# Kernel optimization log

Hardware: AMD Instinct MI355X
Metric: run time of the kernel (lower is better)

The kernel has to match this reference:

```python
import jax, jax.numpy as jnp
import numpy as np

TWN_THRESHOLD_FACTOR = 0.05
BN_EPS = 1e-5


def ternary_quantize(w):
    # threshold = 0.05 * max|w| (detached); q in {-1, 0, +1}
    t = TWN_THRESHOLD_FACTOR * jnp.max(jnp.abs(jax.lax.stop_gradient(w)))
    return (w > t).astype(w.dtype) - (w < -t).astype(w.dtype)


def conv2d(x, w, b):
    q = ternary_quantize(w)
    y = jax.lax.conv_general_dilated(x, q, (1, 1), 'VALID',
                                     dimension_numbers=('NCHW', 'OIHW', 'NCHW'))
    return y + b[None, :, None, None]


def linear(x, w, b):
    q = ternary_quantize(w)
    return x @ q.T + b


def bn_train(x, gamma, beta, axes):
    # training-mode batch norm (biased variance), matches torch BN in train()
    mean = jnp.mean(x, axis=axes, keepdims=True)
    var = jnp.var(x, axis=axes, keepdims=True)
    xhat = (x - mean) * jax.lax.rsqrt(var + BN_EPS)
    shape = [1] * x.ndim
    shape[1] = x.shape[1]
    return xhat * gamma.reshape(shape) + beta.reshape(shape)


def maxpool2(x):
    return jax.lax.reduce_window(x, -jnp.inf, jax.lax.max,
                                 (1, 1, 2, 2), (1, 1, 2, 2), 'VALID')


def setup_inputs() -> dict:
    key = jax.random.key(0)
    ks = jax.random.split(key, 8)
    B, Cin, H, W = 512, 1, 28, 28
    C1, C2, K = 64, 128, 5
    FLAT, F1, F2 = 4 * 4 * C2, 512, 10
    inp = {
        'x': jax.random.normal(ks[0], (B, Cin, H, W), jnp.float32),
        'conv1_w': jax.random.normal(ks[1], (C1, Cin, K, K), jnp.float32) * (1.0 / np.sqrt(Cin * K * K)),
        'conv1_b': jax.random.normal(ks[2], (C1,), jnp.float32) * 0.05,
        'bn1_g': jnp.ones((C1,), jnp.float32),
        'bn1_b': jnp.zeros((C1,), jnp.float32),
        'conv2_w': jax.random.normal(ks[3], (C2, C1, K, K), jnp.float32) * (1.0 / np.sqrt(C1 * K * K)),
        'conv2_b': jax.random.normal(ks[4], (C2,), jnp.float32) * 0.05,
        'bn2_g': jnp.ones((C2,), jnp.float32),
        'bn2_b': jnp.zeros((C2,), jnp.float32),
        'fc1_w': jax.random.normal(ks[5], (F1, FLAT), jnp.float32) * (1.0 / np.sqrt(FLAT)),
        'fc1_b': jax.random.normal(ks[6], (F1,), jnp.float32) * 0.05,
        'bn3_g': jnp.ones((F1,), jnp.float32),
        'bn3_b': jnp.zeros((F1,), jnp.float32),
        'fc2_w': jax.random.normal(ks[7], (F2, F1), jnp.float32) * (1.0 / np.sqrt(F1)),
        'fc2_b': jnp.zeros((F2,), jnp.float32),
    }
    return inp


def reference(x, conv1_w, conv1_b, bn1_g, bn1_b, conv2_w, conv2_b, bn2_g, bn2_b,
              fc1_w, fc1_b, bn3_g, bn3_b, fc2_w, fc2_b):
    h = jax.nn.relu(bn_train(conv2d(x, conv1_w, conv1_b), bn1_g, bn1_b, (0, 2, 3)))
    h = maxpool2(h)  # [B, 64, 12, 12]
    h = jax.nn.relu(bn_train(conv2d(h, conv2_w, conv2_b), bn2_g, bn2_b, (0, 2, 3)))
    h = maxpool2(h)  # [B, 128, 4, 4]
    h = h.reshape(h.shape[0], -1)  # [B, 2048]
    h = jax.nn.relu(bn_train(linear(h, fc1_w, fc1_b), bn3_g, bn3_b, (0,)))
    return linear(h, fc2_w, fc2_b)  # [B, 10]
```

## Files before the change

### kernel.cpp

```cpp
#include <hip/hip_runtime.h>
#include <stdint.h>

#define EPS 1e-5f

typedef short v8s __attribute__((ext_vector_type(8)));
typedef float v4f __attribute__((ext_vector_type(4)));

static const size_t W1F  = 4096;
static const size_t W2F  = 8192;
static const size_t WF2F = 212992;
static const size_t A_F  = 262144;
static const size_t B_F  = 19136512;
static const size_t WF1T = B_F + 1048576;

__device__ inline unsigned short f2bf(float f) {
    unsigned u = __float_as_uint(f);
    return (unsigned short)((u + 0x7FFF + ((u >> 16) & 1)) >> 16);
}

__device__ __forceinline__ void stage16(const unsigned short* g, unsigned short* l) {
    __builtin_amdgcn_global_load_lds(
        (const __attribute__((address_space(1))) unsigned int*)g,
        (__attribute__((address_space(3))) unsigned int*)l, 16, 0, 0);
}

__global__ void k_zero(float* p, int n) {
    int i = blockIdx.x * blockDim.x + threadIdx.x;
    if (i < n) p[i] = 0.f;
}

__global__ void k_absmax4(const float* __restrict__ w0, int n0,
                          const float* __restrict__ w1, int n1,
                          const float* __restrict__ w2, int n2,
                          const float* __restrict__ w3, int n3,
                          float* outv) {
    int blk = blockIdx.x;
    const float* w; int n; unsigned* out; int nb; int bi;
    if (blk < 1)        { w = w0; n = n0; out = (unsigned*)(outv + 0); nb = 1;   bi = blk;      }
    else if (blk < 17)  { w = w1; n = n1; out = (unsigned*)(outv + 1); nb = 16;  bi = blk - 1;  }
    else if (blk < 209) { w = w2; n = n2; out = (unsigned*)(outv + 2); nb = 192; bi = blk - 17; }
    else                { w = w3; n = n3; out = (unsigned*)(outv + 3); nb = 1;   bi = blk - 209; }
    float m = 0.f;
    for (int i = bi * 256 + threadIdx.x; i < n; i += nb * 256)
        m = fmaxf(m, fabsf(w[i]));
    #pragma unroll
    for (int o = 32; o; o >>= 1) m = fmaxf(m, __shfl_down(m, o));
    if ((threadIdx.x & 63) == 0) atomicMax(out, __float_as_uint(m));
}

__global__ void k_quantE(const float* __restrict__ c1w, const float* __restrict__ c2w,
                         const float* __restrict__ f2w, const float* __restrict__ am,
                         float* __restrict__ w1t, unsigned short* __restrict__ w2u,
                         float* __restrict__ wf2) {
    int blk = blockIdx.x;
    if (blk < 1) {
        float t = 0.05f * am[0];
        for (int i = threadIdx.x; i < 1600; i += 256) {
            float v = c1w[i];
            float q = (float)((v > t) - (v < -t));
            int c = i / 25, k = i - c * 25;
            w1t[k * 64 + c] = q;
        }
    } else if (blk < 101) {
        float t = 0.05f * am[1];
        int base = (blk - 1) * 2048;
        #pragma unroll
        for (int jj = 0; jj < 8; ++jj) {
            int i = base + jj * 256 + threadIdx.x;
            int j    = i & 7;
            int lane = (i >> 3) & 63;
            int mt   = (i >> 9) & 7;
            int ks   = (i >> 12) & 1;
            int p    = i >> 13;
            int c  = mt * 16 + (lane & 15);
            int ci = ks * 32 + (lane >> 4) * 8 + j;
            float v = c2w[c * 1600 + ci * 25 + p];
            w2u[i] = (v > t) ? (unsigned short)0x3F80
                             : ((v < -t) ? (unsigned short)0xBF80 : (unsigned short)0);
        }
    } else {
        float t = 0.05f * am[3];
        for (int i = threadIdx.x; i < 5120; i += 256) {
            float v = f2w[i];
            wf2[i] = (float)((v > t) - (v < -t));
        }
    }
}

__global__ void k_quantF1(const float* __restrict__ w, const float* __restrict__ am,
                          unsigned short* __restrict__ wf) {
    float t = 0.05f * am[2];
    int i = blockIdx.x * 256 + threadIdx.x;
    int j    = i & 7;
    int lane = (i >> 3) & 63;
    int ft   = (i >> 9) & 31;
    int ks   = i >> 14;
    int f = ft * 16 + (lane & 15);
    int k = ks * 32 + (lane >> 4) * 8 + j;
    float v = w[f * 2048 + k];
    wf[i] = (v > t) ? (unsigned short)0x3F80
                    : ((v < -t) ? (unsigned short)0xBF80 : (unsigned short)0);
}

__global__ __launch_bounds__(512) void k_conv1(const float* __restrict__ x,
                                               const float* __restrict__ w1t,
                                               unsigned* __restrict__ pmn1,
                                               float* __restrict__ sum,
                                               float* __restrict__ ssq) {
    __shared__ float xs[784];
    __shared__ float red[2][8][64];
    int b = blockIdx.x;
    const float4* xim = (const float4*)(x + (size_t)b * 784);
    for (int i = threadIdx.x; i < 196; i += 512) ((float4*)xs)[i] = xim[i];
    int c  = threadIdx.x & 63;
    int wv = threadIdx.x >> 6;
    float w[25];
    #pragma unroll
    for (int k = 0; k < 25; ++k) w[k] = w1t[k * 64 + c];
    __syncthreads();
    unsigned* ob = pmn1 + (size_t)b * 9216;
    float s = 0.f, s2 = 0.f;
    int ph = 0, pw = wv;
    for (int it = 0; it < 18; ++it) {
        const float* xp = xs + (ph * 2) * 28 + pw * 2;
        float win[36];
        #pragma unroll
        for (int i = 0; i < 6; ++i)
            #pragma unroll
            for (int j = 0; j < 3; ++j) {
                float2 t2 = *(const float2*)(xp + i * 28 + j * 2);
                win[i * 6 + j * 2] = t2.x; win[i * 6 + j * 2 + 1] = t2.y;
            }
        float v00 = 0.f, v01 = 0.f, v10 = 0.f, v11 = 0.f;
        #pragma unroll
        for (int i = 0; i < 5; ++i)
            #pragma unroll
            for (int j = 0; j < 5; ++j) {
                float wk = w[i * 5 + j];
                v00 = fmaf(win[i * 6 + j],           wk, v00);
                v01 = fmaf(win[i * 6 + j + 1],       wk, v01);
                v10 = fmaf(win[(i + 1) * 6 + j],     wk, v10);
                v11 = fmaf(win[(i + 1) * 6 + j + 1], wk, v11);
            }
        s  += v00 + v01 + v10 + v11;
        s2 += v00 * v00 + v01 * v01 + v10 * v10 + v11 * v11;
        float mx = fmaxf(fmaxf(v00, v01), fmaxf(v10, v11));
        float mn = fminf(fminf(v00, v01), fminf(v10, v11));
        ob[(ph * 12 + pw) * 64 + c] = ((unsigned)f2bf(mx) << 16) | (unsigned)f2bf(mn);
        pw += 8; if (pw >= 12) { pw -= 12; ++ph; }
    }
    red[0][wv][c] = s; red[1][wv][c] = s2;
    __syncthreads();
    if (threadIdx.x < 64) {
        float S = 0.f, S2 = 0.f;
        #pragma unroll
        for (int i = 0; i < 8; ++i) { S += red[0][i][threadIdx.x]; S2 += red[1][i][threadIdx.x]; }
        atomicAdd(&sum[threadIdx.x], S);
        atomicAdd(&ssq[threadIdx.x], S2);
    }
}

__global__ void k_bnpool1(const unsigned* __restrict__ pmn1,
                          const float* __restrict__ c1sum, const float* __restrict__ c1ssq,
                          const float* __restrict__ g1, const float* __restrict__ b1,
                          unsigned short* __restrict__ pool1) {
    int i = blockIdx.x * 256 + threadIdx.x;
    int c = i & 63;
    const float invN = 1.f / 294912.f;
    float mean = c1sum[c] * invN;
    float var  = c1ssq[c] * invN - mean * mean;
    float sc = g1[c] * rsqrtf(var + EPS);
    float sh = b1[c] - mean * sc;
    unsigned u = pmn1[i];
    float mx = __uint_as_float(u & 0xffff0000u);
    float mn = __uint_as_float(u << 16);
    float v = (sc > 0.f) ? mx : mn;
    pool1[i] = f2bf(fmaxf(0.f, fmaf(v, sc, sh)));
}

__global__ __launch_bounds__(256) void k_conv2(const unsigned short* __restrict__ pool1,
                                               const unsigned short* __restrict__ wfrag,
                                               float* __restrict__ pmn,
                                               float* __restrict__ sum,
                                               float* __restrict__ ssq) {
    __shared__ unsigned short xs[144 * 76];
    __shared__ unsigned short wb[2][4096];
    __shared__ float reds[2][64], redq[2][64];
    int b     = blockIdx.x >> 1;
    int mhalf = blockIdx.x & 1;
    int tid  = threadIdx.x;
    int lane = tid & 63;
    int wave = tid >> 6;
    const unsigned short* src = pool1 + (size_t)b * 9216;
    for (int i = tid; i < 1152; i += 256) {
        int r = i >> 3, part = i & 7;
        *(float4*)(&xs[r * 76 + part * 8]) = *(const float4*)(src + r * 64 + part * 8);
    }
    #pragma unroll
    for (int h = 0; h < 2; ++h) {
        const unsigned short* g = wfrag + (size_t)(h * 8 + mhalf * 4 + wave) * 512 + lane * 8;
        stage16(g, &wb[0][h * 2048 + wave * 512 + lane * 8]);
    }
    __syncthreads();

    int mh = wave >> 1, nh = wave & 1;
    int n = lane & 15, quad = lane >> 4;
    int ow = n & 7;
    int ohb0 = nh * 4 + (n >> 3);
    int cib  = quad * 8;
    v4f acc[2][2];
    #pragma unroll
    for (int mm = 0; mm < 2; ++mm) { acc[mm][0] = (v4f){0,0,0,0}; acc[mm][1] = (v4f){0,0,0,0}; }
    for (int ss = 0; ss < 25; ++ss) {
        int cur = ss & 1;
        if (ss < 24) {
            #pragma unroll
            for (int h = 0; h < 2; ++h) {
                int st = 2 * ss + 2 + h;
                const unsigned short* g = wfrag +
                    (size_t)(st * 8 + mhalf * 4 + wave) * 512 + lane * 8;
                stage16(g, &wb[cur ^ 1][h * 2048 + wave * 512 + lane * 8]);
            }
        }
        int kh = ss / 5, kw = ss - (ss / 5) * 5;
        #pragma unroll
        for (int ks = 0; ks < 2; ++ks) {
            int col = (ow + kw) * 76 + ks * 32 + cib;
            v8s bf0 = *(const v8s*)(&xs[(ohb0 + kh) * 912 + col]);
            v8s bf1 = *(const v8s*)(&xs[(ohb0 + 2 + kh) * 912 + col]);
            #pragma unroll
            for (int mm = 0; mm < 2; ++mm) {
                v8s af = *(const v8s*)(&wb[cur][ks * 2048 + (mh * 2 + mm) * 512 + lane * 8]);
                acc[mm][0] = __builtin_amdgcn_mfma_f32_16x16x32_bf16(af, bf0, acc[mm][0], 0, 0, 0);
                acc[mm][1] = __builtin_amdgcn_mfma_f32_16x16x32_bf16(af, bf1, acc[mm][1], 0, 0, 0);
            }
        }
        __syncthreads();
    }
    float* po = pmn + (size_t)b * 4096;
    #pragma unroll
    for (int mm = 0; mm < 2; ++mm) {
        int cl0 = (mh * 2 + mm) * 16 + quad * 4;
        #pragma unroll
        for (int r = 0; r < 4; ++r) {
            int cl = cl0 + r;
            int c  = mhalf * 64 + cl;
            float sA = 0.f, s2A = 0.f;
            #pragma unroll
            for (int bf = 0; bf < 2; ++bf) {
                float v = acc[mm][bf][r];
                float pm = fmaxf(v, __shfl_xor(v, 1));
                float pn = fminf(v, __shfl_xor(v, 1));
                pm = fmaxf(pm, __shfl_xor(pm, 8));
                pn = fminf(pn, __shfl_xor(pn, 8));
                if (((n & 1) == 0) && (n < 8)) {
                    int psp = (nh * 2 + bf) * 4 + (n >> 1);
                    *(float2*)(&po[(c * 16 + psp) * 2]) = make_float2(pm, pn);
                }
                float s = v, s2 = v * v;
                #pragma unroll
                for (int m = 1; m < 16; m <<= 1) { s += __shfl_xor(s, m); s2 += __shfl_xor(s2, m); }
                sA += s; s2A += s2;
            }
            if (n == 0) { reds[nh][cl] = sA; redq[nh][cl] = s2A; }
        }
    }
    __syncthreads();
    if (tid < 64) {
        atomicAdd(&sum[mhalf * 64 + tid], reds[0][tid] + reds[1][tid]);
        atomicAdd(&ssq[mhalf * 64 + tid], redq[0][tid] + redq[1][tid]);
    }
}

__global__ void k_bnpool2(const float* __restrict__ pmn, const float* __restrict__ c2sum,
                          const float* __restrict__ c2ssq, const float* __restrict__ g2,
                          const float* __restrict__ b2, unsigned short* __restrict__ xfrag) {
    int i = blockIdx.x * 256 + threadIdx.x;
    int j    = i & 7;
    int lane = (i >> 3) & 63;
    int bt   = (i >> 9) & 31;
    int ks   = i >> 14;
    int b = bt * 16 + (lane & 15);
    int k = ks * 32 + (lane >> 4) * 8 + j;
    int c = k >> 4, psp = k & 15;
    float2 mm = *(const float2*)(&pmn[((size_t)b * 2048 + c * 16 + psp) * 2]);
    float mean = c2sum[c] * (1.f / 32768.f);
    float var  = c2ssq[c] * (1.f / 32768.f) - mean * mean;
    float sc = g2[c] * rsqrtf(var + EPS);
    float sh = b2[c] - mean * sc;
    float v = (sc > 0.f) ? mm.x : mm.y;
    xfrag[i] = f2bf(fmaxf(0.f, fmaf(v, sc, sh)));
}

__global__ __launch_bounds__(256) void k_fc1(const unsigned short* __restrict__ xfrag,
                                             const unsigned short* __restrict__ wfrag,
                                             float* __restrict__ out,
                                             float* __restrict__ sum,
                                             float* __restrict__ ssq) {
    int lane = threadIdx.x & 63;
    int wave = threadIdx.x >> 6;
    int fB = (blockIdx.x & 3) * 8 + wave * 2;
    int bT = blockIdx.x >> 2;
    v4f acc[2];
    acc[0] = (v4f){0,0,0,0}; acc[1] = (v4f){0,0,0,0};
    for (int ks = 0; ks < 64; ++ks) {
        v8s bfrag = *(const v8s*)(xfrag + ((size_t)(ks * 32 + bT) * 64 + lane) * 8);
        #pragma unroll
        for (int mt = 0; mt < 2; ++mt) {
            v8s afrag = *(const v8s*)(wfrag + ((size_t)(ks * 32 + fB + mt) * 64 + lane) * 8);
            acc[mt] = __builtin_amdgcn_mfma_f32_16x16x32_bf16(afrag, bfrag, acc[mt], 0, 0, 0);
        }
    }
    int bb = bT * 16 + (lane & 15);
    int quad = lane >> 4;
    #pragma unroll
    for (int mt = 0; mt < 2; ++mt) {
        int f0 = (fB + mt) * 16 + quad * 4;
        *(float4*)(&out[(size_t)bb * 512 + f0]) =
            make_float4(acc[mt][0], acc[mt][1], acc[mt][2], acc[mt][3]);
        #pragma unroll
        for (int r = 0; r < 4; ++r) {
            float s = acc[mt][r], s2 = s * s;
            #pragma unroll
            for (int m = 1; m < 16; m <<= 1) { s += __shfl_xor(s, m); s2 += __shfl_xor(s2, m); }
            if ((lane & 15) == 0) { atomicAdd(&sum[f0 + r], s); atomicAdd(&ssq[f0 + r], s2); }
        }
    }
}

__global__ __launch_bounds__(256) void k_fc2(const float* __restrict__ x,
                                             const float* __restrict__ w,
                                             const float* __restrict__ bias,
                                             const float* __restrict__ fsum,
                                             const float* __restrict__ fssq,
                                             const float* __restrict__ g3,
                                             const float* __restrict__ b3,
                                             float* __restrict__ out) {
    int lane = threadIdx.x & 63;
    int b = blockIdx.x * 4 + (threadIdx.x >> 6);
    float xa[8], sm[8], sq[8], ga[8], ba[8];
    {
        const float4* p;
        p = (const float4*)(x + (size_t)b * 512 + lane * 8);
        *(float4*)xa = p[0]; *(float4*)(xa + 4) = p[1];
        p = (const float4*)(fsum + lane * 8);
        *(float4*)sm = p[0]; *(float4*)(sm + 4) = p[1];
        p = (const float4*)(fssq + lane * 8);
        *(float4*)sq = p[0]; *(float4*)(sq + 4) = p[1];
        p = (const float4*)(g3 + lane * 8);
        *(float4*)ga = p[0]; *(float4*)(ga + 4) = p[1];
        p = (const float4*)(b3 + lane * 8);
        *(float4*)ba = p[0]; *(float4*)(ba + 4) = p[1];
    }
    float h[8];
    #pragma unroll
    for (int e = 0; e < 8; ++e) {
        float mean = sm[e] * (1.f / 512.f);
        float var  = sq[e] * (1.f / 512.f) - mean * mean;
        float sc = ga[e] * rsqrtf(var + EPS);
        float sh = ba[e] - mean * sc;
        h[e] = fmaxf(0.f, fmaf(xa[e], sc, sh));
    }
    #pragma unroll
    for (int j = 0; j < 10; ++j) {
        const float4* wp = (const float4*)(w + j * 512 + lane * 8);
        float4 w0 = wp[0], w1 = wp[1];
        float p = h[0] * w0.x + h[1] * w0.y + h[2] * w0.z + h[3] * w0.w
                + h[4] * w1.x + h[5] * w1.y + h[6] * w1.z + h[7] * w1.w;
        #pragma unroll
        for (int o = 32; o; o >>= 1) p += __shfl_down(p, o);
        if (lane == 0) out[b * 10 + j] = p + bias[j];
    }
}

extern "C" void kernel_launch(void* const* d_in, const int* in_sizes, int n_in,
                              void* d_out, int out_size, void* d_ws, size_t ws_size,
                              hipStream_t stream) {
    const float* x       = (const float*)d_in[0];
    const float* conv1_w = (const float*)d_in[1];
    const float* bn1_g   = (const float*)d_in[3];
    const float* bn1_b   = (const float*)d_in[4];
    const float* conv2_w = (const float*)d_in[5];
    const float* bn2_g   = (const float*)d_in[7];
    const float* bn2_b   = (const float*)d_in[8];
    const float* fc1_w   = (const float*)d_in[9];
    const float* bn3_g   = (const float*)d_in[11];
    const float* bn3_b   = (const float*)d_in[12];
    const float* fc2_w   = (const float*)d_in[13];
    const float* fc2_b   = (const float*)d_in[14];

    float* wsf = (float*)d_ws;

    float* c1_sum = wsf + 16,   * c1_ssq = wsf + 80;
    float* c2_sum = wsf + 272,  * c2_ssq = wsf + 400;
    float* f_sum  = wsf + 1808, * f_ssq  = wsf + 2320;

    float* w1t = wsf + W1F;
    unsigned short* w2u = (unsigned short*)(wsf + W2F);
    float* wf2 = wsf + WF2F;
    unsigned short* wf1 = (unsigned short*)(wsf + WF1T);
    unsigned* PMN1 = (unsigned*)(wsf + A_F);
    float* PMN2 = wsf + A_F;
    float* A    = wsf + A_F;
    unsigned short* pool1 = (unsigned short*)(wsf + B_F);
    unsigned short* xfrag = (unsigned short*)(wsf + B_F);

    k_zero<<<16, 256, 0, stream>>>(wsf, 4096);

    k_absmax4<<<210, 256, 0, stream>>>(conv1_w, 1600, conv2_w, 204800,
                                       fc1_w, 1048576, fc2_w, 5120, wsf);

    k_quantE<<<102, 256, 0, stream>>>(conv1_w, conv2_w, fc2_w, wsf, w1t, w2u, wf2);

    k_conv1<<<512, 512, 0, stream>>>(x, w1t, PMN1, c1_sum, c1_ssq);

    k_bnpool1<<<18432, 256, 0, stream>>>(PMN1, c1_sum, c1_ssq, bn1_g, bn1_b, pool1);

    k_conv2<<<1024, 256, 0, stream>>>(pool1, w2u, PMN2, c2_sum, c2_ssq);

    k_quantF1<<<4096, 256, 0, stream>>>(fc1_w, wsf, wf1);

    k_bnpool2<<<4096, 256, 0, stream>>>(PMN2, c2_sum, c2_ssq, bn2_g, bn2_b, xfrag);

    k_fc1<<<128, 256, 0, stream>>>(xfrag, wf1, A, f_sum, f_ssq);

    k_fc2<<<128, 256, 0, stream>>>(A, wf2, fc2_b, f_sum, f_ssq, bn3_g, bn3_b,
                                   (float*)d_out);
}
```

Measured before the change: 224.1 us.

## Split conv2 K across waves, coalesce fc1 quantize reads, double fc1 grid

Conv2 now gives each wave all 64 output channels for half of the input-channel K dimension, rather than splitting by M. The two K-halves are reduced through shared memory before the pooling and statistics epilogue, so each B fragment is read once per wave and more MFMAs share it. The fc1 weight quantizer now reads the weights in linear, coalesced order and scatters its writes into fragment layout. The fc1 GEMM assigns one tile per wave and launches twice as many blocks to raise parallelism, at the cost of reloading the activation fragments more often.

```diff
diff --git a/kernel.cpp b/kernel.cpp
--- a/kernel.cpp
+++ b/kernel.cpp
@@ -91,15 +91,14 @@
                           unsigned short* __restrict__ wf) {
     float t = 0.05f * am[2];
     int i = blockIdx.x * 256 + threadIdx.x;
-    int j    = i & 7;
-    int lane = (i >> 3) & 63;
-    int ft   = (i >> 9) & 31;
-    int ks   = i >> 14;
-    int f = ft * 16 + (lane & 15);
-    int k = ks * 32 + (lane >> 4) * 8 + j;
-    float v = w[f * 2048 + k];
-    wf[i] = (v > t) ? (unsigned short)0x3F80
-                    : ((v < -t) ? (unsigned short)0xBF80 : (unsigned short)0);
+    int f = i >> 11, k = i & 2047;
+    float v = w[i];
+    unsigned short q = (v > t) ? (unsigned short)0x3F80
+                     : ((v < -t) ? (unsigned short)0xBF80 : (unsigned short)0);
+    int ft = f >> 4, fm = f & 15;
+    int ks = k >> 5, kr = k & 31;
+    int lane = (kr >> 3) * 16 + fm;
+    wf[((size_t)(ks * 32 + ft) * 64 + lane) * 8 + (kr & 7)] = q;
 }
 
 __global__ __launch_bounds__(512) void k_conv1(const float* __restrict__ x,
@@ -191,6 +190,7 @@
     int tid  = threadIdx.x;
     int lane = tid & 63;
     int wave = tid >> 6;
+    int nh = wave & 1, kp = wave >> 1;
     const unsigned short* src = pool1 + (size_t)b * 9216;
     for (int i = tid; i < 1152; i += 256) {
         int r = i >> 3, part = i & 7;
@@ -198,71 +198,88 @@
     }
     #pragma unroll
     for (int h = 0; h < 2; ++h) {
-        const unsigned short* g = wfrag + (size_t)(h * 8 + mhalf * 4 + wave) * 512 + lane * 8;
-        stage16(g, &wb[0][h * 2048 + wave * 512 + lane * 8]);
+        int ksm = wave * 2 + h;
+        int ks = ksm >> 2, mt = ksm & 3;
+        const unsigned short* g = wfrag + (size_t)(ks * 8 + mhalf * 4 + mt) * 512 + lane * 8;
+        stage16(g, &wb[0][ks * 2048 + mt * 512 + lane * 8]);
     }
     __syncthreads();
 
-    int mh = wave >> 1, nh = wave & 1;
     int n = lane & 15, quad = lane >> 4;
     int ow = n & 7;
     int ohb0 = nh * 4 + (n >> 3);
-    int cib  = quad * 8;
-    v4f acc[2][2];
-    #pragma unroll
-    for (int mm = 0; mm < 2; ++mm) { acc[mm][0] = (v4f){0,0,0,0}; acc[mm][1] = (v4f){0,0,0,0}; }
-    for (int ss = 0; ss < 25; ++ss) {
-        int cur = ss & 1;
-        if (ss < 24) {
+    int col0 = kp * 32 + quad * 8;
+    v4f acc[4][2];
+    #pragma unroll
+    for (int mm = 0; mm < 4; ++mm) { acc[mm][0] = (v4f){0,0,0,0}; acc[mm][1] = (v4f){0,0,0,0}; }
+    for (int p = 0; p < 25; ++p) {
+        int cur = p & 1;
+        if (p < 24) {
             #pragma unroll
             for (int h = 0; h < 2; ++h) {
-                int st = 2 * ss + 2 + h;
+                int ksm = wave * 2 + h;
+                int ks = ksm >> 2, mt = ksm & 3;
                 const unsigned short* g = wfrag +
-                    (size_t)(st * 8 + mhalf * 4 + wave) * 512 + lane * 8;
-                stage16(g, &wb[cur ^ 1][h * 2048 + wave * 512 + lane * 8]);
+                    (size_t)(((p + 1) * 2 + ks) * 8 + mhalf * 4 + mt) * 512 + lane * 8;
+                stage16(g, &wb[cur ^ 1][ks * 2048 + mt * 512 + lane * 8]);
             }
         }
-        int kh = ss / 5, kw = ss - (ss / 5) * 5;
-        #pragma unroll
-        for (int ks = 0; ks < 2; ++ks) {
-            int col = (ow + kw) * 76 + ks * 32 + cib;
-            v8s bf0 = *(const v8s*)(&xs[(ohb0 + kh) * 912 + col]);
-            v8s bf1 = *(const v8s*)(&xs[(ohb0 + 2 + kh) * 912 + col]);
+        int kh = p / 5, kw = p - (p / 5) * 5;
+        int col = (ow + kw) * 76 + col0;
+        v8s bf0 = *(const v8s*)(&xs[(ohb0 + kh) * 912 + col]);
+        v8s bf1 = *(const v8s*)(&xs[(ohb0 + 2 + kh) * 912 + col]);
+        #pragma unroll
+        for (int mm = 0; mm < 4; ++mm) {
+            v8s af = *(const v8s*)(&wb[cur][kp * 2048 + mm * 512 + lane * 8]);
+            acc[mm][0] = __builtin_amdgcn_mfma_f32_16x16x32_bf16(af, bf0, acc[mm][0], 0, 0, 0);
+            acc[mm][1] = __builtin_amdgcn_mfma_f32_16x16x32_bf16(af, bf1, acc[mm][1], 0, 0, 0);
+        }
+        __syncthreads();
+    }
+    float* mbuf = (float*)xs;
+    if (kp == 1) {
+        float* d = mbuf + (nh * 64 + lane) * 36;
+        #pragma unroll
+        for (int mm = 0; mm < 4; ++mm) {
+            *(v4f*)(d + mm * 8)     = acc[mm][0];
+            *(v4f*)(d + mm * 8 + 4) = acc[mm][1];
+        }
+    }
+    __syncthreads();
+    if (kp == 0) {
+        const float* s = mbuf + (nh * 64 + lane) * 36;
+        #pragma unroll
+        for (int mm = 0; mm < 4; ++mm) {
+            acc[mm][0] += *(const v4f*)(s + mm * 8);
+            acc[mm][1] += *(const v4f*)(s + mm * 8 + 4);
+        }
+        float* po = pmn + (size_t)b * 4096;
+        #pragma unroll
+        for (int mm = 0; mm < 4; ++mm) {
+            int cl0 = mm * 16 + quad * 4;
             #pragma unroll
-            for (int mm = 0; mm < 2; ++mm) {
-                v8s af = *(const v8s*)(&wb[cur][ks * 2048 + (mh * 2 + mm) * 512 + lane * 8]);
-                acc[mm][0] = __builtin_amdgcn_mfma_f32_16x16x32_bf16(af, bf0, acc[mm][0], 0, 0, 0);
-                acc[mm][1] = __builtin_amdgcn_mfma_f32_16x16x32_bf16(af, bf1, acc[mm][1], 0, 0, 0);
+            for (int r = 0; r < 4; ++r) {
+                int cl = cl0 + r;
+                int c  = mhalf * 64 + cl;
+                float sA = 0.f, s2A = 0.f;
+                #pragma unroll
+                for (int bf = 0; bf < 2; ++bf) {
+                    float v = acc[mm][bf][r];
+                    float pm = fmaxf(v, __shfl_xor(v, 1));
+                    float pn = fminf(v, __shfl_xor(v, 1));
+                    pm = fmaxf(pm, __shfl_xor(pm, 8));
+                    pn = fminf(pn, __shfl_xor(pn, 8));
+                    if (((n & 1) == 0) && (n < 8)) {
+                        int psp = (nh * 2 + bf) * 4 + (n >> 1);
+                        *(float2*)(&po[(c * 16 + psp) * 2]) = make_float2(pm, pn);
+                    }
+                    float s = v, s2 = v * v;
+                    #pragma unroll
+                    for (int m = 1; m < 16; m <<= 1) { s += __shfl_xor(s, m); s2 += __shfl_xor(s2, m); }
+                    sA += s; s2A += s2;
+                }
+                if (n == 0) { reds[nh][cl] = sA; redq[nh][cl] = s2A; }
             }
-        }
-        __syncthreads();
-    }
-    float* po = pmn + (size_t)b * 4096;
-    #pragma unroll
-    for (int mm = 0; mm < 2; ++mm) {
-        int cl0 = (mh * 2 + mm) * 16 + quad * 4;
-        #pragma unroll
-        for (int r = 0; r < 4; ++r) {
-            int cl = cl0 + r;
-            int c  = mhalf * 64 + cl;
-            float sA = 0.f, s2A = 0.f;
-            #pragma unroll
-            for (int bf = 0; bf < 2; ++bf) {
-                float v = acc[mm][bf][r];
-                float pm = fmaxf(v, __shfl_xor(v, 1));
-                float pn = fminf(v, __shfl_xor(v, 1));
-                pm = fmaxf(pm, __shfl_xor(pm, 8));
-                pn = fminf(pn, __shfl_xor(pn, 8));
-                if (((n & 1) == 0) && (n < 8)) {
-                    int psp = (nh * 2 + bf) * 4 + (n >> 1);
-                    *(float2*)(&po[(c * 16 + psp) * 2]) = make_float2(pm, pn);
-                }
-                float s = v, s2 = v * v;
-                #pragma unroll
-                for (int m = 1; m < 16; m <<= 1) { s += __shfl_xor(s, m); s2 += __shfl_xor(s2, m); }
-                sA += s; s2A += s2;
-            }
-            if (n == 0) { reds[nh][cl] = sA; redq[nh][cl] = s2A; }
         }
     }
     __syncthreads();
@@ -299,32 +316,25 @@
                                              float* __restrict__ ssq) {
     int lane = threadIdx.x & 63;
     int wave = threadIdx.x >> 6;
-    int fB = (blockIdx.x & 3) * 8 + wave * 2;
-    int bT = blockIdx.x >> 2;
-    v4f acc[2];
-    acc[0] = (v4f){0,0,0,0}; acc[1] = (v4f){0,0,0,0};
+    int ft = (blockIdx.x & 7) * 4 + wave;
+    int bT = blockIdx.x >> 3;
+    v4f acc = (v4f){0.f, 0.f, 0.f, 0.f};
     for (int ks = 0; ks < 64; ++ks) {
         v8s bfrag = *(const v8s*)(xfrag + ((size_t)(ks * 32 + bT) * 64 + lane) * 8);
-        #pragma unroll
-        for (int mt = 0; mt < 2; ++mt) {
-            v8s afrag = *(const v8s*)(wfrag + ((size_t)(ks * 32 + fB + mt) * 64 + lane) * 8);
-            acc[mt] = __builtin_amdgcn_mfma_f32_16x16x32_bf16(afrag, bfrag, acc[mt], 0, 0, 0);
-        }
+        v8s afrag = *(const v8s*)(wfrag + ((size_t)(ks * 32 + ft) * 64 + lane) * 8);
+        acc = __builtin_amdgcn_mfma_f32_16x16x32_bf16(afrag, bfrag, acc, 0, 0, 0);
     }
     int bb = bT * 16 + (lane & 15);
     int quad = lane >> 4;
-    #pragma unroll
-    for (int mt = 0; mt < 2; ++mt) {
-        int f0 = (fB + mt) * 16 + quad * 4;
-        *(float4*)(&out[(size_t)bb * 512 + f0]) =
-            make_float4(acc[mt][0], acc[mt][1], acc[mt][2], acc[mt][3]);
-        #pragma unroll
-        for (int r = 0; r < 4; ++r) {
-            float s = acc[mt][r], s2 = s * s;
-            #pragma unroll
-            for (int m = 1; m < 16; m <<= 1) { s += __shfl_xor(s, m); s2 += __shfl_xor(s2, m); }
-            if ((lane & 15) == 0) { atomicAdd(&sum[f0 + r], s); atomicAdd(&ssq[f0 + r], s2); }
-        }
+    int f0 = ft * 16 + quad * 4;
+    *(float4*)(&out[(size_t)bb * 512 + f0]) =
+        make_float4(acc[0], acc[1], acc[2], acc[3]);
+    #pragma unroll
+    for (int r = 0; r < 4; ++r) {
+        float s = acc[r], s2 = s * s;
+        #pragma unroll
+        for (int m = 1; m < 16; m <<= 1) { s += __shfl_xor(s, m); s2 += __shfl_xor(s2, m); }
+        if ((lane & 15) == 0) { atomicAdd(&sum[f0 + r], s); atomicAdd(&ssq[f0 + r], s2); }
     }
 }
 
@@ -422,7 +432,7 @@
 
     k_bnpool2<<<4096, 256, 0, stream>>>(PMN2, c2_sum, c2_ssq, bn2_g, bn2_b, xfrag);
 
-    k_fc1<<<128, 256, 0, stream>>>(xfrag, wf1, A, f_sum, f_ssq);
+    k_fc1<<<256, 256, 0, stream>>>(xfrag, wf1, A, f_sum, f_ssq);
 
     k_fc2<<<128, 256, 0, stream>>>(A, wf2, fc2_b, f_sum, f_ssq, bn3_g, bn3_b,
                                    (float*)d_out);
```

Measured after the change: 214.1 us. 1.05x faster.
